# Performance work log

Hardware: AMD Instinct MI355X
Metric: run time of the kernel (lower is better)

## Reference

```python
import jax, jax.numpy as jnp
from jax import lax
import numpy as np

RATIOS = (0.5, 1.0, 2.0)
SCALES = (8, 16, 32)
BASE = 16
STRIDE = 16
IMG_H, IMG_W = 1024, 1024
NMS_THR = 0.7
N_IN = 6000   # eval mode (training=False)
N_OUT = 300
MIN_SIZE = 16


def _base_anchors():
    ctr = BASE / 2.0
    anc = []
    for r in RATIOS:
        for s in SCALES:
            h = BASE * s * np.sqrt(r)
            w = BASE * s * np.sqrt(1.0 / r)
            anc.append([ctr - h / 2, ctr - w / 2, ctr + h / 2, ctr + w / 2])
    return np.asarray(anc, dtype=np.float32)  # (9,4) yxyx


def _shifted_anchors(H, W):
    base = _base_anchors()
    sy = np.arange(H, dtype=np.float32) * STRIDE
    sx = np.arange(W, dtype=np.float32) * STRIDE
    yy, xx = np.meshgrid(sy, sx, indexing='ij')
    shift = np.stack([yy, xx, yy, xx], axis=-1).reshape(-1, 1, 4)  # (H*W,1,4)
    return jnp.asarray((shift + base[None]).reshape(-1, 4))        # (H*W*9,4)


def _conv(x, w, b):
    y = lax.conv_general_dilated(x, w, (1, 1), 'SAME',
                                 dimension_numbers=('NCHW', 'OIHW', 'NCHW'))
    return y + b[None, :, None, None]


def _loc2bbox(src, locs):
    h = src[:, 2] - src[:, 0]
    w = src[:, 3] - src[:, 1]
    cy = src[:, 0] + 0.5 * h
    cx = src[:, 1] + 0.5 * w
    dy, dx, dh, dw = locs[:, 0], locs[:, 1], locs[:, 2], locs[:, 3]
    cty = dy * h + cy
    ctx = dx * w + cx
    th = jnp.exp(dh) * h
    tw = jnp.exp(dw) * w
    return jnp.stack([cty - 0.5 * th, ctx - 0.5 * tw,
                      cty + 0.5 * th, ctx + 0.5 * tw], axis=-1)


def _nms_keep(boxes, valid):
    n = boxes.shape[0]
    areas = (boxes[:, 2] - boxes[:, 0]) * (boxes[:, 3] - boxes[:, 1])
    idx = jnp.arange(n)

    def body(i, keep):
        b = lax.dynamic_slice(boxes, (i, 0), (1, 4))[0]
        yy1 = jnp.maximum(b[0], boxes[:, 0])
        xx1 = jnp.maximum(b[1], boxes[:, 1])
        yy2 = jnp.minimum(b[2], boxes[:, 2])
        xx2 = jnp.minimum(b[3], boxes[:, 3])
        inter = jnp.clip(yy2 - yy1, 0) * jnp.clip(xx2 - xx1, 0)
        iou = inter / (areas[i] + areas - inter + 1e-9)
        sup = (iou > NMS_THR) & (idx > i) & keep[i]
        return keep & ~sup

    return lax.fori_loop(0, n, body, valid)


def _proposals(locs, fg, anchors):
    # locs (R,4), fg (R,), anchors (R,4) -> (N_OUT,4) padded with zeros
    rois = _loc2bbox(anchors, locs)
    y1 = jnp.clip(rois[:, 0], 0, IMG_H)
    y2 = jnp.clip(rois[:, 2], 0, IMG_H)
    x1 = jnp.clip(rois[:, 1], 0, IMG_W)
    x2 = jnp.clip(rois[:, 3], 0, IMG_W)
    rois = jnp.stack([y1, x1, y2, x2], axis=-1)
    valid = ((y2 - y1) >= MIN_SIZE) & ((x2 - x1) >= MIN_SIZE)
    s = jnp.where(valid, fg, -jnp.inf)
    order = jnp.argsort(-s)[:N_IN]
    rois_s = rois[order]
    valid_s = valid[order]
    keep = _nms_keep(rois_s, valid_s)
    rank = jnp.cumsum(keep.astype(jnp.int32)) - 1
    tgt = jnp.where(keep & (rank < N_OUT), rank, N_OUT)
    out = jnp.zeros((N_OUT + 1, 4), rois.dtype).at[tgt].set(rois_s)
    return out[:N_OUT]


def reference(x, conv_w, conv_b, score_w, score_b, loc_w, loc_b):
    B, C, H, W = x.shape
    anchors = _shifted_anchors(H, W)                      # (R,4)
    h = jax.nn.relu(_conv(x, conv_w, conv_b))             # (B,mid,H,W)
    rpn_locs = _conv(h, loc_w, loc_b).transpose(0, 2, 3, 1).reshape(B, -1, 4)
    rpn_scores = _conv(h, score_w, score_b).transpose(0, 2, 3, 1).reshape(B, -1, 2)
    fg = jax.nn.softmax(rpn_scores, axis=2)[:, :, 1]      # (B,R)
    rois = jax.vmap(_proposals, in_axes=(0, 0, None))(rpn_locs, fg, anchors)
    rois = rois.reshape(-1, 4)                            # (B*N_OUT,4)
    roi_indices = jnp.repeat(jnp.arange(B, dtype=jnp.int32), N_OUT)
    return rpn_scores, rpn_locs, rois, roi_indices, anchors


def setup_inputs() -> dict:
    key = jax.random.key(0)
    ks = jax.random.split(key, 7)
    B, Cin, Cmid, H, W = 4, 512, 512, 64, 64
    return {
        'x': jax.random.normal(ks[0], (B, Cin, H, W), jnp.float32),
        'conv_w': jax.random.normal(ks[1], (Cmid, Cin, 3, 3), jnp.float32) * 0.01,
        'conv_b': jax.random.normal(ks[2], (Cmid,), jnp.float32) * 0.01,
        'score_w': jax.random.normal(ks[3], (18, Cmid, 1, 1), jnp.float32) * 0.01,
        'score_b': jax.random.normal(ks[4], (18,), jnp.float32) * 0.01,
        'loc_w': jax.random.normal(ks[5], (36, Cmid, 1, 1), jnp.float32) * 0.01,
        'loc_b': jax.random.normal(ks[6], (36,), jnp.float32) * 0.01,
    }
```

## Files before the change

### kernel.cpp

```cpp
#include <hip/hip_runtime.h>
#include <cstdint>
#include <cmath>

namespace {
constexpr int BATCH = 4;
constexpr int CIN   = 512;
constexpr int CMID  = 512;
constexpr int HSZ   = 64, WSZ = 64, HWP = 4096;
constexpr int NA    = 36864;
constexpr int NIN_  = 6000;
constexpr int NOUT2 = 300;
constexpr int NW    = 94;

constexpr size_t O_SC  = 0;
constexpr size_t O_LC  = 294912;
constexpr size_t O_ROI = 884736;
constexpr size_t O_IDX = 889536;
constexpr size_t O_ANC = 890736;

constexpr size_t W_H    = 0;
constexpr size_t W_WHI  = 8388608;
constexpr size_t W_WLO  = 9568256;
constexpr size_t W_R4   = 0;
constexpr size_t W_SK   = 589824;
constexpr size_t W_CNT  = 753664;
constexpr size_t W_CUT  = 753668;
constexpr size_t W_CUT2 = 753676;
constexpr size_t W_CUT3 = 753684;
constexpr size_t W_CKEY = 901184;
constexpr size_t W_RS   = 1196096;
constexpr size_t W_VS   = 1292096;
constexpr size_t W_MAT  = 1316096;
}

typedef _Float16 f16;
typedef __attribute__((ext_vector_type(4))) _Float16 f16x4;
typedef __attribute__((ext_vector_type(8))) _Float16 f16x8;
typedef __attribute__((ext_vector_type(4))) float f32x4;

__global__ __launch_bounds__(256) void k0w(const float* __restrict__ w,
                                           f16* __restrict__ whi, f16* __restrict__ wlo) {
    int o = blockIdx.x * 256 + threadIdx.x;
    int ci = o & 511;
    int r  = o >> 9;
    int co = r & 511;
    int kk = r >> 9;
    float f = w[(co * CIN + ci) * 9 + kk] * 64.0f;
    f16 hv = (f16)f;
    whi[o] = hv;
    wlo[o] = (f16)((f - (float)hv) * 2048.0f);
}

__global__ __launch_bounds__(256, 2) void k1_mfma(const float* __restrict__ x,
                                                  const f16* __restrict__ gwh,
                                                  const f16* __restrict__ gwl,
                                                  const float* __restrict__ bias,
                                                  float* __restrict__ h) {
    const int pt = blockIdx.x, cg = blockIdx.y, b = blockIdx.z;
    const int y0 = pt * 2, co0 = cg * 128;
    const int t = threadIdx.x;
    const int wave = t >> 6, lane = t & 63;
    const int wrow = wave >> 1, wco = wave & 1;
    const int m = lane & 15, q = lane >> 4;

    __shared__ __align__(16) f16 xs[2][4 * 66 * 40];
    __shared__ __align__(16) f16 wt[2][2][128 * 32];

    f32x4 acc1[4][4], acc2[4][4];
#pragma unroll
    for (int i = 0; i < 4; ++i)
#pragma unroll
        for (int j = 0; j < 4; ++j) { acc1[i][j] = (f32x4)0.0f; acc2[i][j] = (f32x4)0.0f; }

    const int cq = t & 7, srow = (t >> 3) & 3, cseg = t >> 5;
    const int gy = y0 - 1 + srow;
    const bool yok = (gy >= 0 && gy < HSZ);

    if (t < 128) {
        int buf = t >> 6, rr = (t >> 4) & 3, cc = ((t >> 3) & 1) ? 65 : 0, cq2 = t & 7;
        f16x4 z = (f16x4)(f16)0.0f;
        *(f16x4*)&xs[buf][(rr * 66 + cc) * 40 + cq2 * 4] = z;
    }

    int wbase[2], wpos[2];
#pragma unroll
    for (int s = 0; s < 2; ++s) {
        int idx = s * 256 + t;
        int co_l = idx >> 2, q8 = idx & 3;
        wbase[s] = (co0 + co_l) * 512 + q8 * 8;
        wpos[s]  = co_l * 32 + ((q8 * 8) ^ (((co_l >> 1) & 3) << 3));
    }

#pragma unroll
    for (int s = 0; s < 2; ++s) {
        *(f16x8*)&wt[0][0][wpos[s]] = *(const f16x8*)&gwh[wbase[s]];
        *(f16x8*)&wt[0][1][wpos[s]] = *(const f16x8*)&gwl[wbase[s]];
    }

    const int baseB = wco * 2048 + m * 32 + ((q * 8) ^ (((m >> 1) & 3) << 3));

    int chunk = 0, kk = 0;
    for (int ks = 0; ks < 144; ++ks) {
        const int slot = ks & 1;
        __syncthreads();

        if (kk == 0) {
            float vb[4][8];
            const float* xp = x + ((size_t)(b * CIN + chunk * 32 + cq * 4)) * HWP + gy * WSZ + cseg * 8;
#pragma unroll
            for (int i = 0; i < 4; ++i) {
                if (yok) {
                    float4 u0 = *(const float4*)(xp + (size_t)i * HWP);
                    float4 u1 = *(const float4*)(xp + (size_t)i * HWP + 4);
                    vb[i][0] = u0.x; vb[i][1] = u0.y; vb[i][2] = u0.z; vb[i][3] = u0.w;
                    vb[i][4] = u1.x; vb[i][5] = u1.y; vb[i][6] = u1.z; vb[i][7] = u1.w;
                } else {
#pragma unroll
                    for (int jj = 0; jj < 8; ++jj) vb[i][jj] = 0.0f;
                }
            }
#pragma unroll
            for (int j = 0; j < 8; ++j) {
                int c = (j + cq) & 7;
                int col = cseg * 8 + c + 1;
                f16x4 hv, lv;
#pragma unroll
                for (int i = 0; i < 4; ++i) {
                    float f = vb[i][c];
                    f16 hf = (f16)f;
                    hv[i] = hf;
                    lv[i] = (f16)((f - (float)hf) * 2048.0f);
                }
                int base = (srow * 66 + col) * 40 + cq * 4;
                *(f16x4*)&xs[0][base] = hv;
                *(f16x4*)&xs[1][base] = lv;
            }
        }

        if (ks + 1 < 144) {
            int kk2 = kk + 1, ch2 = chunk;
            if (kk2 == 9) { kk2 = 0; ch2++; }
            const int gofs = kk2 * 262144 + ch2 * 32;
#pragma unroll
            for (int s = 0; s < 2; ++s) {
                int g = wbase[s] + gofs;
                *(f16x8*)&wt[slot ^ 1][0][wpos[s]] = *(const f16x8*)&gwh[g];
                *(f16x8*)&wt[slot ^ 1][1][wpos[s]] = *(const f16x8*)&gwl[g];
            }
        }

        if (kk == 0) __syncthreads();

        const int ky = (kk >= 6) ? 2 : (kk >= 3) ? 1 : 0;
        const int kx = kk - ky * 3;
        const int rs = wrow + ky;

        f16x8 bh[4], bl[4], ah[4], al[4];
#pragma unroll
        for (int nt = 0; nt < 4; ++nt) {
            int off = baseB + nt * 512;
            bh[nt] = *(const f16x8*)&wt[slot][0][off];
            bl[nt] = *(const f16x8*)&wt[slot][1][off];
        }
#pragma unroll
        for (int ct = 0; ct < 4; ++ct) {
            int off = (rs * 66 + ct * 16 + m + kx) * 40 + q * 8;
            ah[ct] = *(const f16x8*)&xs[0][off];
            al[ct] = *(const f16x8*)&xs[1][off];
        }
#pragma unroll
        for (int ct = 0; ct < 4; ++ct)
#pragma unroll
            for (int nt = 0; nt < 4; ++nt) {
                acc1[ct][nt] = __builtin_amdgcn_mfma_f32_16x16x32_f16(ah[ct], bh[nt], acc1[ct][nt], 0, 0, 0);
                acc2[ct][nt] = __builtin_amdgcn_mfma_f32_16x16x32_f16(ah[ct], bl[nt], acc2[ct][nt], 0, 0, 0);
                acc2[ct][nt] = __builtin_amdgcn_mfma_f32_16x16x32_f16(al[ct], bh[nt], acc2[ct][nt], 0, 0, 0);
            }

        ++kk;
        if (kk == 9) { kk = 0; ++chunk; }
    }

    const int y = y0 + wrow;
#pragma unroll
    for (int nt = 0; nt < 4; ++nt) {
        const int co = co0 + wco * 64 + nt * 16 + m;
        const float bv = bias[co];
        size_t rowbase = ((size_t)(b * CMID + co)) * HWP + y * WSZ;
#pragma unroll
        for (int ct = 0; ct < 4; ++ct) {
            float4 o;
            o.x = fmaxf((acc1[ct][nt][0] + acc2[ct][nt][0] * (1.0f / 2048.0f)) * (1.0f / 64.0f) + bv, 0.0f);
            o.y = fmaxf((acc1[ct][nt][1] + acc2[ct][nt][1] * (1.0f / 2048.0f)) * (1.0f / 64.0f) + bv, 0.0f);
            o.z = fmaxf((acc1[ct][nt][2] + acc2[ct][nt][2] * (1.0f / 2048.0f)) * (1.0f / 64.0f) + bv, 0.0f);
            o.w = fmaxf((acc1[ct][nt][3] + acc2[ct][nt][3] * (1.0f / 2048.0f)) * (1.0f / 64.0f) + bv, 0.0f);
            *(float4*)&h[rowbase + ct * 16 + q * 4] = o;
        }
    }
}

__global__ __launch_bounds__(256) void k2_conv1(const float* __restrict__ h,
                                                const float* __restrict__ sw,
                                                const float* __restrict__ sb,
                                                const float* __restrict__ lw,
                                                const float* __restrict__ lb,
                                                float* __restrict__ out) {
    const int y = blockIdx.x;
    const int b = blockIdx.y;
    const int t = threadIdx.x;
    const int c4  = (t & 15) * 4;
    const int px4 = (t >> 4) * 4;
    __shared__ __align__(16) float hs[1024];
    __shared__ __align__(16) float wsm[16 * 68];

    float acc[4][4];
#pragma unroll
    for (int i = 0; i < 4; ++i)
#pragma unroll
        for (int j = 0; j < 4; ++j) acc[i][j] = 0.f;

    const int s_px = (t & 15) * 4;
    const int s_ci = t >> 4;
    for (int ci0 = 0; ci0 < CMID; ci0 += 16) {
        *(float4*)&hs[s_ci * 64 + s_px] =
            *(const float4*)&h[((size_t)(b * CMID + ci0 + s_ci)) * HWP + y * 64 + s_px];
#pragma unroll
        for (int k = 0; k < 4; ++k) {
            int idx = k * 256 + t;
            int ci = idx & 15, c = idx >> 4;
            float v = 0.f;
            if (c < 18) v = sw[c * 512 + ci0 + ci];
            else if (c < 54) v = lw[(c - 18) * 512 + ci0 + ci];
            wsm[ci * 68 + c] = v;
        }
        __syncthreads();
#pragma unroll
        for (int ci = 0; ci < 16; ++ci) {
            float4 hv = *(const float4*)&hs[ci * 64 + px4];
            float4 wv = *(const float4*)&wsm[ci * 68 + c4];
            acc[0][0] = fmaf(wv.x, hv.x, acc[0][0]);
            acc[0][1] = fmaf(wv.x, hv.y, acc[0][1]);
            acc[0][2] = fmaf(wv.x, hv.z, acc[0][2]);
            acc[0][3] = fmaf(wv.x, hv.w, acc[0][3]);
            acc[1][0] = fmaf(wv.y, hv.x, acc[1][0]);
            acc[1][1] = fmaf(wv.y, hv.y, acc[1][1]);
            acc[1][2] = fmaf(wv.y, hv.z, acc[1][2]);
            acc[1][3] = fmaf(wv.y, hv.w, acc[1][3]);
            acc[2][0] = fmaf(wv.z, hv.x, acc[2][0]);
            acc[2][1] = fmaf(wv.z, hv.y, acc[2][1]);
            acc[2][2] = fmaf(wv.z, hv.z, acc[2][2]);
            acc[2][3] = fmaf(wv.z, hv.w, acc[2][3]);
            acc[3][0] = fmaf(wv.w, hv.x, acc[3][0]);
            acc[3][1] = fmaf(wv.w, hv.y, acc[3][1]);
            acc[3][2] = fmaf(wv.w, hv.z, acc[3][2]);
            acc[3][3] = fmaf(wv.w, hv.w, acc[3][3]);
        }
        __syncthreads();
    }

#pragma unroll
    for (int cc = 0; cc < 4; ++cc) {
        int c = c4 + cc;
        if (c >= 54) break;
        float bv = (c < 18) ? sb[c] : lb[c - 18];
#pragma unroll
        for (int pp = 0; pp < 4; ++pp) {
            int px = y * 64 + px4 + pp;
            float v = acc[cc][pp] + bv;
            if (c < 18)
                out[O_SC + (size_t)b * 73728 + (size_t)px * 18 + c] = v;
            else
                out[O_LC + (size_t)b * 147456 + (size_t)px * 36 + (c - 18)] = v;
        }
    }
}

__global__ __launch_bounds__(256) void k3_prop(float* __restrict__ out,
                                               float* __restrict__ rois4,
                                               float* __restrict__ skey) {
    const int t = threadIdx.x;
    const int p = blockIdx.x * 256 + t;
    const int b = blockIdx.y;
    const int px = p / 9;
    const int a  = p - px * 9;
    const int yy = px >> 6, xx = px & 63;
    const int ri = a / 3, si = a - ri * 3;
    const double rat[3] = {0.5, 1.0, 2.0};
    const double scl[3] = {8.0, 16.0, 32.0};
    double hhd = 16.0 * scl[si] * sqrt(rat[ri]);
    double wwd = 16.0 * scl[si] * sqrt(1.0 / rat[ri]);
    float a0 = (float)(8.0 - hhd / 2.0), a1 = (float)(8.0 - wwd / 2.0);
    float a2 = (float)(8.0 + hhd / 2.0), a3 = (float)(8.0 + wwd / 2.0);
    float sy = (float)(yy * 16), sx = (float)(xx * 16);
    float A0 = sy + a0, A1 = sx + a1, A2 = sy + a2, A3 = sx + a3;
    if (b == 0) {
        float4 av; av.x = A0; av.y = A1; av.z = A2; av.w = A3;
        *(float4*)&out[O_ANC + (size_t)p * 4] = av;
    }
    const float* sc = out + O_SC + (size_t)b * 73728 + (size_t)px * 18 + a * 2;
    float s0 = sc[0], s1 = sc[1];
    float mm = fmaxf(s0, s1);
    float e0 = expf(s0 - mm), e1 = expf(s1 - mm);
    float fg = e1 / (e0 + e1);
    const float* lc = out + O_LC + (size_t)b * 147456 + (size_t)px * 36 + a * 4;
    float dy = lc[0], dxv = lc[1], dh = lc[2], dwv = lc[3];
    float ah = A2 - A0, aw = A3 - A1;
    float cy = A0 + 0.5f * ah, cx = A1 + 0.5f * aw;
    float cty = dy * ah + cy, ctx = dxv * aw + cx;
    float th = expf(dh) * ah, tw = expf(dwv) * aw;
    float ry1 = cty - 0.5f * th, rx1 = ctx - 0.5f * tw;
    float ry2 = cty + 0.5f * th, rx2 = ctx + 0.5f * tw;
    float y1 = fminf(fmaxf(ry1, 0.f), 1024.f);
    float y2 = fminf(fmaxf(ry2, 0.f), 1024.f);
    float x1 = fminf(fmaxf(rx1, 0.f), 1024.f);
    float x2 = fminf(fmaxf(rx2, 0.f), 1024.f);
    bool valid = ((y2 - y1) >= 16.f) && ((x2 - x1) >= 16.f);
    float sk = valid ? fg : -__builtin_inff();
    float4 rv; rv.x = y1; rv.y = x1; rv.z = y2; rv.w = x2;
    *(float4*)&rois4[((size_t)b * NA + p) * 4] = rv;
    skey[(size_t)b * NA + p] = sk;
}

__global__ __launch_bounds__(1024) void k4r(const float* __restrict__ skey,
                                            int* __restrict__ cut1g,
                                            int* __restrict__ cut2g,
                                            int* __restrict__ cut3g) {
    const int b = blockIdx.x, t = threadIdx.x;
    const int w8 = (t >> 6) & 7;
    __shared__ int h8[8][4096];
    __shared__ int tsum[256];
    __shared__ int s_cut, s_prev;
    int cum = 0;
    int cuts[3];
#pragma unroll 1
    for (int level = 0; level < 3; ++level) {
        for (int k = t; k < 8 * 4096; k += 1024) ((int*)h8)[k] = 0;
        __syncthreads();
        for (int i = t; i < NA; i += 1024) {
            float sk = skey[(size_t)b * NA + i];
            unsigned u = __float_as_uint(sk);
            u = (u & 0x80000000u) ? ~u : (u | 0x80000000u);
            int b1 = (int)(u >> 20), b2 = (int)((u >> 8) & 0xFFFu);
            int digit; bool pred;
            if (level == 0)      { digit = b1;                pred = true; }
            else if (level == 1) { digit = b2;                pred = (b1 == cuts[0]); }
            else                 { digit = (36863 - i) >> 4;  pred = (b1 == cuts[0] && b2 == cuts[1]); }
            if (pred) atomicAdd(&h8[w8][digit], 1);
        }
        __syncthreads();
        for (int k = t; k < 4096; k += 1024) {
            int s = h8[0][k];
#pragma unroll
            for (int r = 1; r < 8; ++r) s += h8[r][k];
            h8[0][k] = s;
        }
        __syncthreads();
        if (t < 256) {
            int s = 0;
#pragma unroll
            for (int j = 0; j < 16; ++j) s += h8[0][t * 16 + j];
            tsum[t] = s;
        }
        __syncthreads();
        if (t == 0) {
            int run = 0;
            for (int tt = 255; tt >= 0; --tt) { int tmp = tsum[tt]; tsum[tt] = run; run += tmp; }
        }
        __syncthreads();
        if (t < 256) {
            const int target = NIN_ - cum;
            int run = tsum[t];
            for (int v = t * 16 + 15; v >= t * 16; --v) {
                int prev = run;
                run += h8[0][v];
                if (run >= target && prev < target) { s_cut = v; s_prev = prev; }
            }
        }
        __syncthreads();
        cuts[level] = s_cut;
        cum += s_prev;
        __syncthreads();
    }
    if (t == 0) { cut1g[b] = cuts[0]; cut2g[b] = cuts[1]; cut3g[b] = cuts[2]; }
}

__global__ __launch_bounds__(256) void k4c_compact(const float* __restrict__ skey,
                                                   const int* __restrict__ cut1,
                                                   const int* __restrict__ cut2,
                                                   const int* __restrict__ cut3,
                                                   int* __restrict__ cnt,
                                                   unsigned long long* __restrict__ ckey) {
    const int p = blockIdx.x * 256 + threadIdx.x;
    const int b = blockIdx.y;
    float sk = skey[(size_t)b * NA + p];
    unsigned u = __float_as_uint(sk);
    u = (u & 0x80000000u) ? ~u : (u | 0x80000000u);
    int b1 = (int)(u >> 20), b2 = (int)((u >> 8) & 0xFFFu), b3 = (36863 - p) >> 4;
    int c1 = cut1[b], c2 = cut2[b], c3 = cut3[b];
    bool take = (b1 > c1) || (b1 == c1 && (b2 > c2 || (b2 == c2 && b3 >= c3)));
    if (take) {
        int pos = atomicAdd(&cnt[b], 1);
        ckey[(size_t)b * NA + pos] =
            ((unsigned long long)u << 16) | (unsigned long long)(36863 - p);
    }
}

__global__ __launch_bounds__(1024) void k4d_sort(const int* __restrict__ cnt,
                                                 const unsigned long long* __restrict__ ckey,
                                                 const float* __restrict__ rois4,
                                                 float* __restrict__ rois_s,
                                                 int* __restrict__ valid_s) {
    const int b = blockIdx.x, t = threadIdx.x;
    const int C = min(cnt[b], 8192);
    __shared__ unsigned long long keys[8192];
#pragma unroll
    for (int s = 0; s < 8; ++s) {
        int i = s * 1024 + t;
        keys[i] = (i < C) ? ckey[(size_t)b * NA + i] : 0ull;
    }
    __syncthreads();
    for (int k = 2; k <= 8192; k <<= 1) {
        for (int j = k >> 1; j > 0; j >>= 1) {
#pragma unroll
            for (int s = 0; s < 8; ++s) {
                int i = s * 1024 + t;
                int ixj = i ^ j;
                if (ixj > i) {
                    unsigned long long x = keys[i], y = keys[ixj];
                    bool up = ((i & k) == 0);
                    if (up ? (x < y) : (x > y)) { keys[i] = y; keys[ixj] = x; }
                }
            }
            __syncthreads();
        }
    }
    for (int r = t; r < NIN_; r += 1024) {
        unsigned long long key = keys[r];
        int p = 36863 - (int)(key & 0xFFFFull);
        const float4 bx = *(const float4*)&rois4[((size_t)b * NA + p) * 4];
        *(float4*)&rois_s[((size_t)b * NIN_ + r) * 4] = bx;
        valid_s[b * NIN_ + r] = ((unsigned)(key >> 16) != 0x007FFFFFu) ? 1 : 0;
    }
}

__global__ __launch_bounds__(256) void k5_mat(const float* __restrict__ rois_s,
                                              unsigned long long* __restrict__ mat) {
    const int b = blockIdx.y, rb = blockIdx.x;
    const int t = threadIdx.x, wave = t >> 6, lane = t & 63;
    const int i = rb * 64 + lane;
    const bool rowok = (i < NIN_);
    __shared__ float cs[4][5][64];
    const float* bb = rois_s + (size_t)b * NIN_ * 4;

    float r0 = 0, r1 = 0, r2 = 0, r3 = 0, ra = 0;
    if (rowok) {
        float4 v = *(const float4*)&bb[(size_t)i * 4];
        r0 = v.x; r1 = v.y; r2 = v.z; r3 = v.w;
        ra = (v.z - v.x) * (v.w - v.y);
    }
    unsigned long long* mrow = mat + ((size_t)b * NIN_ + (size_t)(rowok ? i : 0)) * NW;

    if (rowok)
        for (int cb = wave; cb < rb; cb += 4) mrow[cb] = 0ull;

    for (int cb = rb + wave; cb < NW; cb += 4) {
        const int j0 = cb * 64;
        const int j  = j0 + lane;
        float4 v;
        if (j < NIN_) v = *(const float4*)&bb[(size_t)j * 4];
        else { v.x = 0; v.y = 0; v.z = 0; v.w = 0; }
        cs[wave][0][lane] = v.x; cs[wave][1][lane] = v.y;
        cs[wave][2][lane] = v.z; cs[wave][3][lane] = v.w;
        cs[wave][4][lane] = (v.z - v.x) * (v.w - v.y);
        unsigned long long wm = 0;
        if (rowok) {
#pragma unroll 8
            for (int k = 0; k < 64; ++k) {
                float yy1 = fmaxf(r0, cs[wave][0][k]), xx1 = fmaxf(r1, cs[wave][1][k]);
                float yy2 = fminf(r2, cs[wave][2][k]), xx2 = fminf(r3, cs[wave][3][k]);
                float inter = fmaxf(yy2 - yy1, 0.f) * fmaxf(xx2 - xx1, 0.f);
                float iou = inter / (ra + cs[wave][4][k] - inter + 1e-9f);
                int jj = j0 + k;
                if ((iou > 0.7f) && (jj > i) && (jj < NIN_)) wm |= (1ull << k);
            }
            mrow[cb] = wm;
        }
    }
}

__global__ __launch_bounds__(64) void k5_scan(const unsigned long long* __restrict__ mat,
                                              const float* __restrict__ rois_s,
                                              const int* __restrict__ valid_s,
                                              float* __restrict__ out) {
    const int b = blockIdx.x, t = threadIdx.x;
    for (int k = t; k < NOUT2 * 4; k += 64) out[O_ROI + (size_t)b * NOUT2 * 4 + k] = 0.f;
    for (int k = t; k < NOUT2; k += 64) out[O_IDX + (size_t)b * NOUT2 + k] = (float)b;

    unsigned long long A = 0, B = 0;
    for (int w = 0; w < NW; ++w) {
        int i = w * 64 + t;
        int v = (i < NIN_) ? valid_s[b * NIN_ + i] : 0;
        unsigned long long m = __ballot(v == 0);
        if (w < 64) { if (t == w) A = m; }
        else        { if (t == w - 64) B = m; }
    }

    const unsigned long long* mb = mat + (size_t)b * NIN_ * NW;
    const float* bb = rois_s + (size_t)b * NIN_ * 4;
    int kept = 0;
    for (int w = 0; w < NW && kept < NOUT2; ++w) {
        unsigned long long cur = (w < 64) ? __shfl(A, w) : __shfl(B, w - 64);
        unsigned long long avail = ~cur;
        while (avail != 0ull && kept < NOUT2) {
            int bit = __builtin_ctzll(avail);
            int i = w * 64 + bit;
            if (t == 0) {
                float4 bx = *(const float4*)&bb[(size_t)i * 4];
                *(float4*)&out[O_ROI + ((size_t)b * NOUT2 + kept) * 4] = bx;
            }
            kept++;
            if (kept >= NOUT2) break;
            const unsigned long long* row = mb + (size_t)i * NW;
            unsigned long long rA = row[t];
            unsigned long long rB = (t < NW - 64) ? row[64 + t] : 0ull;
            A |= rA; B |= rB;
            unsigned long long rw = (w < 64) ? __shfl(rA, w) : __shfl(rB, w - 64);
            avail &= ~rw;
            avail &= ~(1ull << bit);
        }
    }
}

extern "C" void kernel_launch(void* const* d_in, const int* in_sizes, int n_in,
                              void* d_out, int out_size, void* d_ws, size_t ws_size,
                              hipStream_t stream) {
    const float* x       = (const float*)d_in[0];
    const float* conv_w  = (const float*)d_in[1];
    const float* conv_b  = (const float*)d_in[2];
    const float* score_w = (const float*)d_in[3];
    const float* score_b = (const float*)d_in[4];
    const float* loc_w   = (const float*)d_in[5];
    const float* loc_b   = (const float*)d_in[6];
    float* out = (float*)d_out;
    float* ws  = (float*)d_ws;

    f16* whi = (f16*)(ws + W_WHI);
    f16* wlo = (f16*)(ws + W_WLO);

    k0w<<<2359296 / 256, 256, 0, stream>>>(conv_w, whi, wlo);
    k1_mfma<<<dim3(32, 4, 4), 256, 0, stream>>>(x, whi, wlo, conv_b, ws + W_H);
    k2_conv1<<<dim3(64, 4), 256, 0, stream>>>(ws + W_H, score_w, score_b, loc_w, loc_b, out);
    hipMemsetAsync(ws + W_CNT, 0, 128, stream);
    k3_prop<<<dim3(144, 4), 256, 0, stream>>>(out, ws + W_R4, ws + W_SK);
    k4r<<<BATCH, 1024, 0, stream>>>(ws + W_SK, (int*)(ws + W_CUT),
                                    (int*)(ws + W_CUT2), (int*)(ws + W_CUT3));
    k4c_compact<<<dim3(144, 4), 256, 0, stream>>>(ws + W_SK, (const int*)(ws + W_CUT),
                                                  (const int*)(ws + W_CUT2),
                                                  (const int*)(ws + W_CUT3),
                                                  (int*)(ws + W_CNT),
                                                  (unsigned long long*)(ws + W_CKEY));
    k4d_sort<<<BATCH, 1024, 0, stream>>>((const int*)(ws + W_CNT),
                                         (const unsigned long long*)(ws + W_CKEY),
                                         ws + W_R4, ws + W_RS, (int*)(ws + W_VS));
    k5_mat<<<dim3(NW, BATCH), 256, 0, stream>>>(ws + W_RS, (unsigned long long*)(ws + W_MAT));
    k5_scan<<<BATCH, 64, 0, stream>>>((const unsigned long long*)(ws + W_MAT),
                                      ws + W_RS, (const int*)(ws + W_VS), out);
}
```

Measured before the change: 978.0 us.

## Pre-split input to fp16 hi/lo layout; replace bitonic sort with rank scatter

A new pre-pass kernel converts x once into a channel-interleaved fp16 hi/lo layout, so the conv kernel loads packed f16x8 values and no longer converts fp32 per tile. The radix-cut and compaction kernels are merged into one block-per-batch kernel with a shared-memory counter, which removes the memset and a launch. The single-block bitonic sort is replaced by a multi-block rank-by-counting kernel that scatters each key to its position. These are meant to cut conversion work in the conv hot loop and the serial sort latency, at the cost of an extra 32MB of workspace traffic and O(C^2) comparisons.

New measurement: 894.6 us. 8.5% less time.

```diff
diff --git a/kernel.cpp b/kernel.cpp
--- a/kernel.cpp
+++ b/kernel.cpp
@@ -21,12 +21,11 @@
 constexpr size_t W_H    = 0;
 constexpr size_t W_WHI  = 8388608;
 constexpr size_t W_WLO  = 9568256;
+constexpr size_t W_XSP  = 10747904;
+constexpr size_t W_END_PS = 19136512;
 constexpr size_t W_R4   = 0;
 constexpr size_t W_SK   = 589824;
 constexpr size_t W_CNT  = 753664;
-constexpr size_t W_CUT  = 753668;
-constexpr size_t W_CUT2 = 753676;
-constexpr size_t W_CUT3 = 753684;
 constexpr size_t W_CKEY = 901184;
 constexpr size_t W_RS   = 1196096;
 constexpr size_t W_VS   = 1292096;
@@ -51,7 +50,38 @@
     wlo[o] = (f16)((f - (float)hv) * 2048.0f);
 }
 
+__global__ __launch_bounds__(256) void k0x(const float* __restrict__ x,
+                                           f16* __restrict__ xsp) {
+    const int pt = blockIdx.x, ch = blockIdx.y, b = blockIdx.z, t = threadIdx.x;
+    __shared__ float ld[32 * 261];
+    const int px0 = pt * 256;
+    const int lpx = (t & 63) * 4, lc0 = t >> 6;
+#pragma unroll
+    for (int r = 0; r < 8; ++r) {
+        int ci = r * 4 + lc0;
+        float4 v = *(const float4*)&x[((size_t)(b * 512 + ch * 32 + ci)) * 4096 + px0 + lpx];
+        float* d = &ld[ci * 261 + lpx];
+        d[0] = v.x; d[1] = v.y; d[2] = v.z; d[3] = v.w;
+    }
+    __syncthreads();
+    size_t ob = ((size_t)(b * 16 + ch) * 4096 + px0 + t) * 64;
+#pragma unroll
+    for (int cqx = 0; cqx < 8; ++cqx) {
+        f16x8 o;
+#pragma unroll
+        for (int i = 0; i < 4; ++i) {
+            float f = ld[(cqx * 4 + i) * 261 + t];
+            f16 hf = (f16)f;
+            o[i]     = hf;
+            o[4 + i] = (f16)((f - (float)hf) * 2048.0f);
+        }
+        *(f16x8*)&xsp[ob + cqx * 8] = o;
+    }
+}
+
+template <bool PS>
 __global__ __launch_bounds__(256, 2) void k1_mfma(const float* __restrict__ x,
+                                                  const f16* __restrict__ xsp,
                                                   const f16* __restrict__ gwh,
                                                   const f16* __restrict__ gwl,
                                                   const float* __restrict__ bias,
@@ -90,7 +120,6 @@
         wbase[s] = (co0 + co_l) * 512 + q8 * 8;
         wpos[s]  = co_l * 32 + ((q8 * 8) ^ (((co_l >> 1) & 3) << 3));
     }
-
 #pragma unroll
     for (int s = 0; s < 2; ++s) {
         *(f16x8*)&wt[0][0][wpos[s]] = *(const f16x8*)&gwh[wbase[s]];
@@ -105,35 +134,49 @@
         __syncthreads();
 
         if (kk == 0) {
-            float vb[4][8];
-            const float* xp = x + ((size_t)(b * CIN + chunk * 32 + cq * 4)) * HWP + gy * WSZ + cseg * 8;
-#pragma unroll
-            for (int i = 0; i < 4; ++i) {
-                if (yok) {
-                    float4 u0 = *(const float4*)(xp + (size_t)i * HWP);
-                    float4 u1 = *(const float4*)(xp + (size_t)i * HWP + 4);
-                    vb[i][0] = u0.x; vb[i][1] = u0.y; vb[i][2] = u0.z; vb[i][3] = u0.w;
-                    vb[i][4] = u1.x; vb[i][5] = u1.y; vb[i][6] = u1.z; vb[i][7] = u1.w;
-                } else {
-#pragma unroll
-                    for (int jj = 0; jj < 8; ++jj) vb[i][jj] = 0.0f;
+            if (PS) {
+                const f16* xb = xsp + (((size_t)(b * 16 + chunk) * 4096 + (size_t)(gy < 0 ? 0 : gy) * 64) * 64);
+#pragma unroll
+                for (int j = 0; j < 8; ++j) {
+                    int c = (j + cq) & 7;
+                    int col = cseg * 8 + c + 1;
+                    f16x8 v = (f16x8)(f16)0.0f;
+                    if (yok) v = *(const f16x8*)&xb[(size_t)(cseg * 8 + c) * 64 + cq * 8];
+                    int base = (srow * 66 + col) * 40 + cq * 4;
+                    *(f16x4*)&xs[0][base] = __builtin_shufflevector(v, v, 0, 1, 2, 3);
+                    *(f16x4*)&xs[1][base] = __builtin_shufflevector(v, v, 4, 5, 6, 7);
                 }
-            }
-#pragma unroll
-            for (int j = 0; j < 8; ++j) {
-                int c = (j + cq) & 7;
-                int col = cseg * 8 + c + 1;
-                f16x4 hv, lv;
+            } else {
+                float vb[4][8];
+                const float* xp = x + ((size_t)(b * CIN + chunk * 32 + cq * 4)) * HWP + gy * WSZ + cseg * 8;
 #pragma unroll
                 for (int i = 0; i < 4; ++i) {
-                    float f = vb[i][c];
-                    f16 hf = (f16)f;
-                    hv[i] = hf;
-                    lv[i] = (f16)((f - (float)hf) * 2048.0f);
+                    if (yok) {
+                        float4 u0 = *(const float4*)(xp + (size_t)i * HWP);
+                        float4 u1 = *(const float4*)(xp + (size_t)i * HWP + 4);
+                        vb[i][0] = u0.x; vb[i][1] = u0.y; vb[i][2] = u0.z; vb[i][3] = u0.w;
+                        vb[i][4] = u1.x; vb[i][5] = u1.y; vb[i][6] = u1.z; vb[i][7] = u1.w;
+                    } else {
+#pragma unroll
+                        for (int jj = 0; jj < 8; ++jj) vb[i][jj] = 0.0f;
+                    }
                 }
-                int base = (srow * 66 + col) * 40 + cq * 4;
-                *(f16x4*)&xs[0][base] = hv;
-                *(f16x4*)&xs[1][base] = lv;
+#pragma unroll
+                for (int j = 0; j < 8; ++j) {
+                    int c = (j + cq) & 7;
+                    int col = cseg * 8 + c + 1;
+                    f16x4 hv, lv;
+#pragma unroll
+                    for (int i = 0; i < 4; ++i) {
+                        float f = vb[i][c];
+                        f16 hf = (f16)f;
+                        hv[i] = hf;
+                        lv[i] = (f16)((f - (float)hf) * 2048.0f);
+                    }
+                    int base = (srow * 66 + col) * 40 + cq * 4;
+                    *(f16x4*)&xs[0][base] = hv;
+                    *(f16x4*)&xs[1][base] = lv;
+                }
             }
         }
 
@@ -321,15 +364,14 @@
     skey[(size_t)b * NA + p] = sk;
 }
 
-__global__ __launch_bounds__(1024) void k4r(const float* __restrict__ skey,
-                                            int* __restrict__ cut1g,
-                                            int* __restrict__ cut2g,
-                                            int* __restrict__ cut3g) {
+__global__ __launch_bounds__(1024) void k4rc(const float* __restrict__ skey,
+                                             int* __restrict__ cnt,
+                                             unsigned long long* __restrict__ ckey) {
     const int b = blockIdx.x, t = threadIdx.x;
     const int w8 = (t >> 6) & 7;
     __shared__ int h8[8][4096];
     __shared__ int tsum[256];
-    __shared__ int s_cut, s_prev;
+    __shared__ int s_cut, s_prev, lcnt;
     int cum = 0;
     int cuts[3];
 #pragma unroll 1
@@ -381,65 +423,64 @@
         cum += s_prev;
         __syncthreads();
     }
-    if (t == 0) { cut1g[b] = cuts[0]; cut2g[b] = cuts[1]; cut3g[b] = cuts[2]; }
-}
-
-__global__ __launch_bounds__(256) void k4c_compact(const float* __restrict__ skey,
-                                                   const int* __restrict__ cut1,
-                                                   const int* __restrict__ cut2,
-                                                   const int* __restrict__ cut3,
-                                                   int* __restrict__ cnt,
-                                                   unsigned long long* __restrict__ ckey) {
-    const int p = blockIdx.x * 256 + threadIdx.x;
+    if (t == 0) lcnt = 0;
+    __syncthreads();
+    const int c1 = cuts[0], c2 = cuts[1], c3 = cuts[2];
+    for (int i = t; i < NA; i += 1024) {
+        float sk = skey[(size_t)b * NA + i];
+        unsigned u = __float_as_uint(sk);
+        u = (u & 0x80000000u) ? ~u : (u | 0x80000000u);
+        int b1 = (int)(u >> 20), b2 = (int)((u >> 8) & 0xFFFu), b3 = (36863 - i) >> 4;
+        bool take = (b1 > c1) || (b1 == c1 && (b2 > c2 || (b2 == c2 && b3 >= c3)));
+        if (take) {
+            int pos = atomicAdd(&lcnt, 1);
+            ckey[(size_t)b * NA + pos] =
+                ((unsigned long long)u << 16) | (unsigned long long)(36863 - i);
+        }
+    }
+    __syncthreads();
+    if (t == 0) cnt[b] = lcnt;
+}
+
+__global__ __launch_bounds__(256) void k4d_rank(const int* __restrict__ cnt,
+                                                const unsigned long long* __restrict__ ckey,
+                                                const float* __restrict__ rois4,
+                                                float* __restrict__ rois_s,
+                                                int* __restrict__ valid_s) {
     const int b = blockIdx.y;
-    float sk = skey[(size_t)b * NA + p];
-    unsigned u = __float_as_uint(sk);
-    u = (u & 0x80000000u) ? ~u : (u | 0x80000000u);
-    int b1 = (int)(u >> 20), b2 = (int)((u >> 8) & 0xFFFu), b3 = (36863 - p) >> 4;
-    int c1 = cut1[b], c2 = cut2[b], c3 = cut3[b];
-    bool take = (b1 > c1) || (b1 == c1 && (b2 > c2 || (b2 == c2 && b3 >= c3)));
-    if (take) {
-        int pos = atomicAdd(&cnt[b], 1);
-        ckey[(size_t)b * NA + pos] =
-            ((unsigned long long)u << 16) | (unsigned long long)(36863 - p);
-    }
-}
-
-__global__ __launch_bounds__(1024) void k4d_sort(const int* __restrict__ cnt,
-                                                 const unsigned long long* __restrict__ ckey,
-                                                 const float* __restrict__ rois4,
-                                                 float* __restrict__ rois_s,
-                                                 int* __restrict__ valid_s) {
-    const int b = blockIdx.x, t = threadIdx.x;
-    const int C = min(cnt[b], 8192);
-    __shared__ unsigned long long keys[8192];
-#pragma unroll
-    for (int s = 0; s < 8; ++s) {
-        int i = s * 1024 + t;
-        keys[i] = (i < C) ? ckey[(size_t)b * NA + i] : 0ull;
-    }
-    __syncthreads();
-    for (int k = 2; k <= 8192; k <<= 1) {
-        for (int j = k >> 1; j > 0; j >>= 1) {
-#pragma unroll
-            for (int s = 0; s < 8; ++s) {
-                int i = s * 1024 + t;
-                int ixj = i ^ j;
-                if (ixj > i) {
-                    unsigned long long x = keys[i], y = keys[ixj];
-                    bool up = ((i & k) == 0);
-                    if (up ? (x < y) : (x > y)) { keys[i] = y; keys[ixj] = x; }
-                }
+    const int C = cnt[b];
+    if (blockIdx.x * 256 >= C) return;
+    const int gi = blockIdx.x * 256 + threadIdx.x;
+    const bool act = gi < C;
+    const unsigned long long mk = act ? ckey[(size_t)b * NA + gi] : 0ULL;
+    __shared__ unsigned long long kl[512];
+    int rank = 0;
+    for (int c0 = 0; c0 < C; c0 += 512) {
+        __syncthreads();
+#pragma unroll
+        for (int kk = 0; kk < 2; ++kk) {
+            int k = threadIdx.x + kk * 256;
+            int src = c0 + k;
+            kl[k] = (src < C) ? ckey[(size_t)b * NA + src] : 0ULL;
+        }
+        __syncthreads();
+        if (act) {
+            int n = min(512, C - c0);
+            int j = 0;
+            for (; j + 4 <= n; j += 4) {
+                rank += (kl[j]     > mk);
+                rank += (kl[j + 1] > mk);
+                rank += (kl[j + 2] > mk);
+                rank += (kl[j + 3] > mk);
             }
-            __syncthreads();
-        }
-    }
-    for (int r = t; r < NIN_; r += 1024) {
-        unsigned long long key = keys[r];
-        int p = 36863 - (int)(key & 0xFFFFull);
+            for (; j < n; ++j) rank += (kl[j] > mk);
+        }
+    }
+    if (act && rank < NIN_) {
+        int p = 36863 - (int)(mk & 0xFFFFull);
         const float4 bx = *(const float4*)&rois4[((size_t)b * NA + p) * 4];
-        *(float4*)&rois_s[((size_t)b * NIN_ + r) * 4] = bx;
-        valid_s[b * NIN_ + r] = ((unsigned)(key >> 16) != 0x007FFFFFu) ? 1 : 0;
+        *(float4*)&rois_s[((size_t)b * NIN_ + rank) * 4] = bx;
+        valid_s[b * NIN_ + rank] = ((unsigned)(mk >> 16) != 0x007FFFFFu) ? 1 : 0;
     }
 }
 
@@ -546,22 +587,23 @@
 
     f16* whi = (f16*)(ws + W_WHI);
     f16* wlo = (f16*)(ws + W_WLO);
+    f16* xsp = (f16*)(ws + W_XSP);
+    const bool ps = (ws_size >= (size_t)W_END_PS * 4);
 
     k0w<<<2359296 / 256, 256, 0, stream>>>(conv_w, whi, wlo);
-    k1_mfma<<<dim3(32, 4, 4), 256, 0, stream>>>(x, whi, wlo, conv_b, ws + W_H);
+    if (ps) {
+        k0x<<<dim3(16, 16, 4), 256, 0, stream>>>(x, xsp);
+        k1_mfma<true><<<dim3(32, 4, 4), 256, 0, stream>>>(x, xsp, whi, wlo, conv_b, ws + W_H);
+    } else {
+        k1_mfma<false><<<dim3(32, 4, 4), 256, 0, stream>>>(x, nullptr, whi, wlo, conv_b, ws + W_H);
+    }
     k2_conv1<<<dim3(64, 4), 256, 0, stream>>>(ws + W_H, score_w, score_b, loc_w, loc_b, out);
-    hipMemsetAsync(ws + W_CNT, 0, 128, stream);
     k3_prop<<<dim3(144, 4), 256, 0, stream>>>(out, ws + W_R4, ws + W_SK);
-    k4r<<<BATCH, 1024, 0, stream>>>(ws + W_SK, (int*)(ws + W_CUT),
-                                    (int*)(ws + W_CUT2), (int*)(ws + W_CUT3));
-    k4c_compact<<<dim3(144, 4), 256, 0, stream>>>(ws + W_SK, (const int*)(ws + W_CUT),
-                                                  (const int*)(ws + W_CUT2),
-                                                  (const int*)(ws + W_CUT3),
-                                                  (int*)(ws + W_CNT),
-                                                  (unsigned long long*)(ws + W_CKEY));
-    k4d_sort<<<BATCH, 1024, 0, stream>>>((const int*)(ws + W_CNT),
-                                         (const unsigned long long*)(ws + W_CKEY),
-                                         ws + W_R4, ws + W_RS, (int*)(ws + W_VS));
+    k4rc<<<BATCH, 1024, 0, stream>>>(ws + W_SK, (int*)(ws + W_CNT),
+                                     (unsigned long long*)(ws + W_CKEY));
+    k4d_rank<<<dim3(24, BATCH), 256, 0, stream>>>((const int*)(ws + W_CNT),
+                                                  (const unsigned long long*)(ws + W_CKEY),
+                                                  ws + W_R4, ws + W_RS, (int*)(ws + W_VS));
     k5_mat<<<dim3(NW, BATCH), 256, 0, stream>>>(ws + W_RS, (unsigned long long*)(ws + W_MAT));
     k5_scan<<<BATCH, 64, 0, stream>>>((const unsigned long long*)(ws + W_MAT),
                                       ws + W_RS, (const int*)(ws + W_VS), out);
```
